# Kernel optimization log

Hardware: AMD Instinct MI355X
Metric: run time of the kernel (lower is better)

Reference implementation:

```python
import jax, jax.numpy as jnp
import numpy as np

EPS = 1e-5
B, S, D = 4, 2048, 128
BALL_SCALE = 0.05  # keeps points inside the unit Poincare ball for c=1


def setup_inputs() -> dict:
    key = jax.random.key(0)
    kq, kk, kv = jax.random.split(key, 3)
    q = jax.random.normal(kq, (B, S, D), dtype=jnp.float32) * BALL_SCALE
    k = jax.random.normal(kk, (B, S, D), dtype=jnp.float32) * BALL_SCALE
    v_tangent = jax.random.normal(kv, (B, S, D), dtype=jnp.float32)
    c = jnp.asarray(1.0, dtype=jnp.float32)
    beta = jnp.asarray(0.0, dtype=jnp.float32)            # nn.Parameter init 0.0
    attention_bias = jnp.asarray(0.0, dtype=jnp.float32)  # nn.Parameter init 0.0
    return {"q": q, "k": k, "v_tangent": v_tangent, "c": c,
            "beta": beta, "attention_bias": attention_bias}


def reference(q, k, v_tangent, c, beta, attention_bias):
    sqrt_c = jnp.sqrt(c)

    # --- pairwise Poincare distance (all fp32, as in the torch autocast block) ---
    x_norm_sq = jnp.sum(q * q, axis=-1, keepdims=True)            # (B,S,1)
    y_norm_sq = jnp.sum(k * k, axis=-1, keepdims=True)            # (B,S,1)
    xy_dot = jnp.einsum('bsd,btd->bst', q, k)                     # (B,S,S)
    y_norm_sq_t = jnp.swapaxes(y_norm_sq, -2, -1)                 # (B,1,S)
    diff_norm_sq = x_norm_sq - 2.0 * xy_dot + y_norm_sq_t         # ||x-y||^2, (B,S,S)
    denom = (1.0 - c * x_norm_sq) * (1.0 - c * y_norm_sq_t)       # (B,S,S)
    arg = 1.0 + 2.0 * c * diff_norm_sq / jnp.maximum(denom, EPS)
    dist = jnp.arccosh(jnp.maximum(arg, 1.0 + EPS)) / sqrt_c      # (B,S,S)

    # --- attention ---
    beta_positive = jax.nn.softplus(beta)
    attention_scores = -beta_positive * dist - attention_bias
    attention_weights = jax.nn.softmax(attention_scores, axis=-1)  # (B,S,S)
    output_tangent = jnp.einsum('bst,btd->bsd', attention_weights, v_tangent)

    # --- exp map at origin ---
    v_norm = jnp.maximum(
        jnp.sqrt(jnp.sum(output_tangent * output_tangent, axis=-1, keepdims=True)), EPS)
    output_hyperbolic = (jnp.tanh(sqrt_c * v_norm) / sqrt_c) * (output_tangent / v_norm)

    return output_hyperbolic, attention_weights
```

## Files before the change

kernel.cpp:

```cpp
#include <hip/hip_runtime.h>
#include <math.h>

#define B_ 4
#define S_ 2048
#define D_ 128
#define EPSF 1e-5f
#define BN 128
#define PSB 272
#define PRS 4112

typedef __attribute__((ext_vector_type(8))) short short8;
typedef __attribute__((ext_vector_type(4))) float f32x4;

static __device__ __forceinline__ unsigned short f2bf(float f) {
    unsigned u = __float_as_uint(f);
    return (unsigned short)((u + 0x7fffu + ((u >> 16) & 1u)) >> 16);
}


__global__ __launch_bounds__(256) void convqk_kernel(const float* __restrict__ q,
                                                     const float* __restrict__ k,
                                                     const float* __restrict__ cp,
                                                     float* __restrict__ qn, float* __restrict__ kn,
                                                     float* __restrict__ lws,
                                                     float2* __restrict__ qng, float2* __restrict__ kng,
                                                     unsigned* __restrict__ Qb, unsigned* __restrict__ Kb) {
    int row = blockIdx.x * 4 + (threadIdx.x >> 6);
    int lane = threadIdx.x & 63;
    const int NR = B_ * S_;
    const float cc = cp[0];
    bool isQ = row < NR;
    int r = isQ ? row : row - NR;
    float2 v = ((const float2*)(isQ ? q : k))[(size_t)r * 64 + lane];
    unsigned pk = (unsigned)f2bf(v.x) | ((unsigned)f2bf(v.y) << 16);
    float nrm = v.x * v.x + v.y * v.y;
#pragma unroll
    for (int m = 1; m <= 32; m <<= 1) nrm += __shfl_xor(nrm, m, 64);
    if (isQ) {
        Qb[(size_t)r * 64 + lane] = pk;
        if (lane == 0) {
            qn[r] = nrm;
            qng[r] = make_float2(nrm, 2.f * cc * __builtin_amdgcn_rcpf(1.f - cc * nrm));
        }
        if (lane == 1) lws[r] = 0.f;
    } else {
        int c = lane >> 2;
        int cs = c ^ (r & 7);
        Kb[(size_t)r * 64 + cs * 4 + (lane & 3)] = pk;
        if (lane == 0) {
            kn[r] = nrm;
            kng[r] = make_float2(nrm, __builtin_amdgcn_rcpf(1.f - cc * nrm));
        }
    }
}

__global__ __launch_bounds__(256) void convv_kernel(const float* __restrict__ v, uint4* __restrict__ Vtb) {
    __shared__ unsigned short Vs[128 * 132];
    int b = blockIdx.x >> 4;
    int t = blockIdx.x & 15;
    int tid = threadIdx.x;
    const float* src = v + ((size_t)b * S_ + t * 128) * D_;
    int d4 = tid & 31, key0 = tid >> 5;
#pragma unroll
    for (int it = 0; it < 16; ++it) {
        int key = key0 + it * 8;
        float4 f = *(const float4*)(src + (size_t)key * D_ + d4 * 4);
        unsigned short* dst = &Vs[key * 132 + d4 * 4];
        dst[0] = f2bf(f.x); dst[1] = f2bf(f.y); dst[2] = f2bf(f.z); dst[3] = f2bf(f.w);
    }
    __syncthreads();
    uint4* tile = Vtb + (size_t)blockIdx.x * (128 * 16);
    int d = tid & 127;
    int cl = tid >> 7;
#pragma unroll
    for (int it = 0; it < 8; ++it) {
        int c = cl + it * 2;
        int kb = c * 8;
        unsigned short e0 = Vs[(kb + 0) * 132 + d], e1 = Vs[(kb + 1) * 132 + d];
        unsigned short e2 = Vs[(kb + 2) * 132 + d], e3 = Vs[(kb + 3) * 132 + d];
        unsigned short e4 = Vs[(kb + 4) * 132 + d], e5 = Vs[(kb + 5) * 132 + d];
        unsigned short e6 = Vs[(kb + 6) * 132 + d], e7 = Vs[(kb + 7) * 132 + d];
        uint4 o;
        o.x = (unsigned)e0 | ((unsigned)e1 << 16);
        o.y = (unsigned)e2 | ((unsigned)e3 << 16);
        o.z = (unsigned)e4 | ((unsigned)e5 << 16);
        o.w = (unsigned)e6 | ((unsigned)e7 << 16);
        tile[d * 16 + (c ^ (d & 7))] = o;
    }
}


__global__ __launch_bounds__(1024, 4) void hattn6_kernel(
    const unsigned short* __restrict__ Qb, const char* __restrict__ Kb, const char* __restrict__ Vtb,
    const float2* __restrict__ qng, const float2* __restrict__ kng,
    const float* __restrict__ cp, const float* __restrict__ betap, const float* __restrict__ biasp,
    float* __restrict__ hout, float* __restrict__ wout) {

    __shared__ __align__(1024) char smem[132096];
    float* l_row = (float*)(smem + 131840);
    float* nsq_s = (float*)(smem + 131968);

    const int tid = threadIdx.x;
    const int lane = tid & 63, wave = tid >> 6;
    const int wm = wave & 1, wn = wave >> 1;
    const int lm = lane & 15, quad = lane >> 4;

    int xcd = blockIdx.x & 7;
    int b = xcd >> 1;
    int rb = (blockIdx.x >> 3) * 2 + (xcd & 1);
    int s0 = rb * 32;
    const size_t bS = (size_t)b * S_;

    const float beta = betap[0], bias = biasp[0];
    const float cc = cp[0];
    const float beta_pos = fmaxf(beta, 0.f) + log1pf(__expf(-fabsf(beta)));
    const float sqrt_c = sqrtf(cc);
    const float bneg = -beta_pos / sqrt_c;
    const float bias2 = -bias * 1.442695040888963f;
    const float onepe = 1.f + EPSF;

    const char* KbBase = Kb + bS * 256;
    const char* VtBase = Vtb + (size_t)b * 16 * 32768;

    if (tid < 32) {
        float2 x = qng[bS + s0 + tid];
        *(float2*)(smem + 131584 + tid * 8) = x;
    } else if (tid < 64) {
        l_row[tid - 32] = 0.f;
    } else if (tid < 96) {
        nsq_s[tid - 64] = 0.f;
    }

    const int n0 = wn * 16 + lm;
    short8 kf[4];
    float2 yg;
    {
        const char* kb0 = KbBase + n0 * 256;
#pragma unroll
        for (int ks = 0; ks < 4; ++ks) {
            int c = ks * 4 + quad;
            kf[ks] = *(const short8*)(kb0 + ((c ^ (n0 & 7)) * 16));
        }
        yg = kng[bS + n0];
    }

    short8 aq[4];
    {
        const unsigned short* qrow = Qb + (bS + s0 + wm * 16 + lm) * D_;
#pragma unroll
        for (int ks = 0; ks < 4; ++ks)
            aq[ks] = *(const short8*)(qrow + ks * 32 + quad * 8);
    }

    __syncthreads();

    float2 xr4[4];
#pragma unroll
    for (int r = 0; r < 4; ++r)
        xr4[r] = *(const float2*)(smem + 131584 + (wm * 16 + quad * 4 + r) * 8);

    f32x4 o = {0.f, 0.f, 0.f, 0.f};
    float lacc[4] = {0.f, 0.f, 0.f, 0.f};

    for (int it = 0; it < 16; ++it) {
        f32x4 acc = {0.f, 0.f, 0.f, 0.f};
#pragma unroll
        for (int ks = 0; ks < 4; ++ks)
            acc = __builtin_amdgcn_mfma_f32_16x16x32_bf16(aq[ks], kf[ks], acc, 0, 0, 0);

        short8 kfn[4];
        float2 ygn;
        if (it < 15) {
            const char* kb = KbBase + (size_t)(it + 1) * 32768 + n0 * 256;
#pragma unroll
            for (int ks = 0; ks < 4; ++ks) {
                int c = ks * 4 + quad;
                kfn[ks] = *(const short8*)(kb + ((c ^ (n0 & 7)) * 16));
            }
            ygn = kng[bS + (size_t)(it + 1) * 128 + n0];
        }

        short8 vf[4];
        {
            const char* vb = VtBase + (size_t)it * 32768 + n0 * 256;
#pragma unroll
            for (int ks = 0; ks < 4; ++ks) {
                int c = ks * 4 + quad;
                vf[ks] = *(const short8*)(vb + ((c ^ (n0 & 7)) * 16));
            }
        }

#pragma unroll
        for (int r = 0; r < 4; ++r) {
            int row = wm * 16 + quad * 4 + r;
            float diff = fmaf(-2.f, acc[r], xr4[r].x + yg.x);
            float arg = fmaf(diff * yg.y, xr4[r].y, 1.f);
            arg = fmaxf(arg, onepe);
            float w = arg + sqrtf(fmaf(arg, arg, -1.f));
            float pv = __builtin_amdgcn_exp2f(fmaf(bneg, __builtin_amdgcn_logf(w), bias2));
            *(unsigned short*)(smem + row * PRS + (it * 128 + n0) * 2) = f2bf(pv);
            lacc[r] += pv;
        }
        __syncthreads();

        {
            const char* prow = smem + (wm * 16 + lm) * PRS + it * 256 + quad * 16;
#pragma unroll
            for (int ks = 0; ks < 4; ++ks) {
                short8 ap = *(const short8*)(prow + ks * 64);
                o = __builtin_amdgcn_mfma_f32_16x16x32_bf16(ap, vf[ks], o, 0, 0, 0);
            }
        }

        if (it < 15) {
#pragma unroll
            for (int ks = 0; ks < 4; ++ks) kf[ks] = kfn[ks];
            yg = ygn;
        }
    }

#pragma unroll
    for (int r = 0; r < 4; ++r) {
        float s = lacc[r];
#pragma unroll
        for (int m = 1; m <= 8; m <<= 1) s += __shfl_xor(s, m, 64);
        if (lm == 0) atomicAdd(&l_row[wm * 16 + quad * 4 + r], s);
    }
    __syncthreads();

    float linv[4];
#pragma unroll
    for (int r = 0; r < 4; ++r) linv[r] = 1.f / l_row[wm * 16 + quad * 4 + r];

#pragma unroll
    for (int r = 0; r < 4; ++r) {
        float x = o[r] * linv[r];
        o[r] = x;
        float np = x * x;
#pragma unroll
        for (int m = 1; m <= 8; m <<= 1) np += __shfl_xor(np, m, 64);
        if (lm == 0) atomicAdd(&nsq_s[wm * 16 + quad * 4 + r], np);
    }
    __syncthreads();
#pragma unroll
    for (int r = 0; r < 4; ++r) {
        int row = wm * 16 + quad * 4 + r;
        float vn = fmaxf(sqrtf(nsq_s[row]), EPSF);
        float a = sqrt_c * vn;
        float th = 1.f - 2.f / (__expf(2.f * a) + 1.f);
        float sc = th / a;
        hout[(bS + s0 + row) * D_ + n0] = o[r] * sc;
    }

    {
        float4* wdst = (float4*)(wout + (bS + s0) * (size_t)S_);
#pragma unroll
        for (int j = 0; j < 8; ++j) {
            int idx = tid + j * 1024;
            int row = idx >> 8;
            int ch = idx & 255;
            float lr = 1.f / l_row[row];
            uint4 u = *(const uint4*)(smem + row * PRS + ch * 16);
            float4 f0, f1;
            f0.x = __uint_as_float(u.x << 16) * lr;
            f0.y = __uint_as_float(u.x & 0xffff0000u) * lr;
            f0.z = __uint_as_float(u.y << 16) * lr;
            f0.w = __uint_as_float(u.y & 0xffff0000u) * lr;
            f1.x = __uint_as_float(u.z << 16) * lr;
            f1.y = __uint_as_float(u.z & 0xffff0000u) * lr;
            f1.z = __uint_as_float(u.w << 16) * lr;
            f1.w = __uint_as_float(u.w & 0xffff0000u) * lr;
            wdst[idx * 2] = f0;
            wdst[idx * 2 + 1] = f1;
        }
    }
}


__global__ __launch_bounds__(512, 2) void hattn_kernel(
    const unsigned short* __restrict__ Qb, const char* __restrict__ Kb, const char* __restrict__ Vtb,
    const float* __restrict__ qn, const float* __restrict__ kn,
    const float* __restrict__ cp, const float* __restrict__ betap, const float* __restrict__ biasp,
    float* __restrict__ lws, float* __restrict__ houtg, float* __restrict__ woutg) {

    __shared__ __align__(1024) char smem[75136];
    char* KsB = smem;
    char* VtB = smem + 32768;
    char* PsB = smem + 65536;
    float* kn_s  = (float*)(smem + 74240);
    float* qn_s  = (float*)(smem + 74752);
    float* l_row = (float*)(smem + 74880);
    float* nsq_s = (float*)(smem + 75008);

    const int tid = threadIdx.x;
    const int lane = tid & 63, wave = tid >> 6;
    const int wm = wave & 1, wn = wave >> 1;
    const int lm = lane & 15, quad = lane >> 4;

    int xcd = blockIdx.x & 7;
    int b = xcd >> 1;
    int rb = (blockIdx.x >> 3) * 2 + (xcd & 1);
    int s0 = rb * 32;
    const size_t bS = (size_t)b * S_;

    const float cc = cp[0], beta = betap[0], bias = biasp[0];
    const float beta_pos = fmaxf(beta, 0.f) + log1pf(__expf(-fabsf(beta)));
    const float sqrt_c = sqrtf(cc);
    const float inv_sqrt_c = 1.f / sqrt_c;

    if (tid < 32) {
        qn_s[tid] = qn[bS + s0 + tid];
        l_row[tid] = 0.f;
        nsq_s[tid] = 0.f;
    }

    short8 aq[4];
    {
        const unsigned short* qrow = Qb + (bS + s0 + wm * 16 + lm) * D_;
#pragma unroll
        for (int ks = 0; ks < 4; ++ks)
            aq[ks] = *(const short8*)(qrow + ks * 32 + quad * 8);
    }

    f32x4 o0 = {0.f, 0.f, 0.f, 0.f}, o1 = {0.f, 0.f, 0.f, 0.f};

    const char* KbBase = Kb + bS * 256;
    const char* VtBase = Vtb + (size_t)b * 16 * 32768;

    for (int t = 0; t < S_ / BN; ++t) {
        int t0 = t * BN;
        __syncthreads();
        {
            const uint4* ksrc = (const uint4*)(KbBase + (size_t)t0 * 256);
            const uint4* vsrc = (const uint4*)(VtBase + (size_t)t * 32768);
            uint4* kd = (uint4*)KsB;
            uint4* vd = (uint4*)VtB;
#pragma unroll
            for (int i = 0; i < 4; ++i) {
                kd[tid + i * 512] = ksrc[tid + i * 512];
                vd[tid + i * 512] = vsrc[tid + i * 512];
            }
            if (tid < BN) kn_s[tid] = kn[bS + t0 + tid];
        }
        __syncthreads();

        f32x4 acc0 = {0.f, 0.f, 0.f, 0.f}, acc1 = {0.f, 0.f, 0.f, 0.f};
#pragma unroll
        for (int ks = 0; ks < 4; ++ks) {
            int n0 = wn * 32 + lm;
            int c = ks * 4 + quad;
            short8 b0 = *(const short8*)(KsB + n0 * 256 + ((c ^ (n0 & 7)) * 16));
            int n1 = n0 + 16;
            short8 b1 = *(const short8*)(KsB + n1 * 256 + ((c ^ (n1 & 7)) * 16));
            acc0 = __builtin_amdgcn_mfma_f32_16x16x32_bf16(aq[ks], b0, acc0, 0, 0, 0);
            acc1 = __builtin_amdgcn_mfma_f32_16x16x32_bf16(aq[ks], b1, acc1, 0, 0, 0);
        }

        float lp[4];
#pragma unroll
        for (int r = 0; r < 4; ++r) {
            int row = wm * 16 + quad * 4 + r;
            float xn = qn_s[row];
            float fx = 1.f - cc * xn;
            float p0, p1;
#pragma unroll
            for (int nt = 0; nt < 2; ++nt) {
                int col = wn * 32 + nt * 16 + lm;
                float dot = (nt == 0) ? acc0[r] : acc1[r];
                float yn = kn_s[col];
                float diff = xn - 2.f * dot + yn;
                float den = fmaxf(fx * (1.f - cc * yn), EPSF);
                float arg = fmaf(2.f * cc * diff, __builtin_amdgcn_rcpf(den), 1.f);
                arg = fmaxf(arg, 1.f + EPSF);
                float dist = __logf(arg + sqrtf(arg * arg - 1.f)) * inv_sqrt_c;
                float p = __expf(fmaf(-beta_pos, dist, -bias));
                woutg[(bS + s0 + row) * S_ + t0 + col] = p;
                *(unsigned short*)(PsB + row * PSB + col * 2) = f2bf(p);
                if (nt == 0) p0 = p; else p1 = p;
            }
            lp[r] = p0 + p1;
        }
#pragma unroll
        for (int r = 0; r < 4; ++r) {
            float s = lp[r];
#pragma unroll
            for (int m = 1; m <= 8; m <<= 1) s += __shfl_xor(s, m, 64);
            if (lm == 0) atomicAdd(&l_row[wm * 16 + quad * 4 + r], s);
        }
        __syncthreads();

#pragma unroll
        for (int ks = 0; ks < 4; ++ks) {
            short8 ap = *(const short8*)(PsB + (wm * 16 + lm) * PSB + (ks * 32 + quad * 8) * 2);
            int d0 = wn * 32 + lm;
            int c = ks * 4 + quad;
            short8 v0 = *(const short8*)(VtB + d0 * 256 + ((c ^ (d0 & 7)) * 16));
            int d1 = d0 + 16;
            short8 v1 = *(const short8*)(VtB + d1 * 256 + ((c ^ (d1 & 7)) * 16));
            o0 = __builtin_amdgcn_mfma_f32_16x16x32_bf16(ap, v0, o0, 0, 0, 0);
            o1 = __builtin_amdgcn_mfma_f32_16x16x32_bf16(ap, v1, o1, 0, 0, 0);
        }
    }
    __syncthreads();

    float xs0[4], xs1[4];
#pragma unroll
    for (int r = 0; r < 4; ++r) {
        int row = wm * 16 + quad * 4 + r;
        float linv = __builtin_amdgcn_rcpf(l_row[row]);
        float x0 = o0[r] * linv, x1 = o1[r] * linv;
        xs0[r] = x0; xs1[r] = x1;
        float np = x0 * x0 + x1 * x1;
#pragma unroll
        for (int m = 1; m <= 8; m <<= 1) np += __shfl_xor(np, m, 64);
        if (lm == 0) atomicAdd(&nsq_s[row], np);
    }
    if (tid < 32) lws[bS + s0 + tid] = l_row[tid];
    __syncthreads();
#pragma unroll
    for (int r = 0; r < 4; ++r) {
        int row = wm * 16 + quad * 4 + r;
        float vn = fmaxf(sqrtf(nsq_s[row]), EPSF);
        float a = sqrt_c * vn;
        float th = 1.f - 2.f * __builtin_amdgcn_rcpf(__expf(2.f * a) + 1.f);
        float sc = th / a;
        houtg[(bS + s0 + row) * D_ + wn * 32 + lm] = xs0[r] * sc;
        houtg[(bS + s0 + row) * D_ + wn * 32 + 16 + lm] = xs1[r] * sc;
    }
}

__global__ __launch_bounds__(256) void wnorm_kernel(float* __restrict__ w,
                                                    const float* __restrict__ lws) {
    size_t idx = (size_t)blockIdx.x * 256 + threadIdx.x;
    int row = (int)(idx >> 9);
    float linv = 1.f / lws[row];
    float4* p = (float4*)w + idx;
    float4 v = *p;
    v.x *= linv; v.y *= linv; v.z *= linv; v.w *= linv;
    *p = v;
}


extern "C" void kernel_launch(void* const* d_in, const int* in_sizes, int n_in,
                              void* d_out, int out_size, void* d_ws, size_t ws_size,
                              hipStream_t stream) {
    const float* q    = (const float*)d_in[0];
    const float* k    = (const float*)d_in[1];
    const float* v    = (const float*)d_in[2];
    const float* c    = (const float*)d_in[3];
    const float* beta = (const float*)d_in[4];
    const float* ab   = (const float*)d_in[5];

    float* out  = (float*)d_out;
    float* hout = out;
    float* wout = out + (size_t)B_ * S_ * D_;

    float* qn  = (float*)d_ws;
    float* kn  = qn + B_ * S_;
    float* lws = kn + B_ * S_;
    char*  wsb = (char*)d_ws;
    const size_t QG_OFF = 98304;
    const size_t KG_OFF = QG_OFF + 65536;
    const size_t QB_OFF = KG_OFF + 65536;
    const size_t KB_OFF = QB_OFF + 2097152;
    const size_t VT_OFF = KB_OFF + 2097152;
    const size_t NEED1  = VT_OFF + 2097152;

    float2*  qng = (float2*)(wsb + QG_OFF);
    float2*  kng = (float2*)(wsb + KG_OFF);
    unsigned* Qb = (unsigned*)(wsb + QB_OFF);
    unsigned* Kb = (unsigned*)(wsb + KB_OFF);
    uint4*   Vtb = (uint4*)(wsb + VT_OFF);

    if (ws_size >= NEED1) {
        convqk_kernel<<<4096, 256, 0, stream>>>(q, k, c, qn, kn, lws, qng, kng, Qb, Kb);
        convv_kernel<<<64, 256, 0, stream>>>(v, Vtb);
        hattn6_kernel<<<256, 1024, 0, stream>>>((const unsigned short*)Qb, (const char*)Kb,
                                                (const char*)Vtb, qng, kng, c, beta, ab,
                                                hout, wout);
    } else {
        convqk_kernel<<<4096, 256, 0, stream>>>(q, k, c, qn, kn, lws, qng, kng, Qb, Kb);
        convv_kernel<<<64, 256, 0, stream>>>(v, Vtb);
        hattn_kernel<<<256, 512, 0, stream>>>((const unsigned short*)Qb, (const char*)Kb,
                                              (const char*)Vtb, qn, kn, c, beta, ab,
                                              lws, hout, wout);
        wnorm_kernel<<<(B_ * S_ * S_ / 4) / 256, 256, 0, stream>>>(wout, lws);
    }
}
```

Measured before the change: 136.8 us.

## Re-layout K and V bf16 tiles into k-slice-major order for coalesced fragment loads

Changes the workspace layout of the bf16 K and transposed V tiles from XOR-swizzled rows to a k-slice-major layout (ks*8192 + n*64 + quad*16), so each wave's MFMA fragment loads hit contiguous 1 KB segments instead of strided 256-byte rows. It also hoists the V and next-K global loads to the top of the loop behind a sched_barrier so they issue before the QK MFMAs, and pads the P row stride in shared memory. The fallback kernel is updated to match the new layout. The intent is to cut global-load transaction count and latency in the main attention kernel, at the cost of higher register pressure from the early loads.

```diff
diff --git a/kernel.cpp b/kernel.cpp
--- a/kernel.cpp
+++ b/kernel.cpp
@@ -7,7 +7,7 @@
 #define EPSF 1e-5f
 #define BN 128
 #define PSB 272
-#define PRS 4112
+#define PRS 4128
 
 typedef __attribute__((ext_vector_type(8))) short short8;
 typedef __attribute__((ext_vector_type(4))) float f32x4;
@@ -44,9 +44,10 @@
         }
         if (lane == 1) lws[r] = 0.f;
     } else {
-        int c = lane >> 2;
-        int cs = c ^ (r & 7);
-        Kb[(size_t)r * 64 + cs * 4 + (lane & 3)] = pk;
+        int b = r >> 11, rbk = r & 2047;
+        int tile = rbk >> 7, n = rbk & 127;
+        Kb[(size_t)b * 131072 + tile * 8192 + (lane >> 4) * 2048 + n * 16 +
+           ((lane >> 2) & 3) * 4 + (lane & 3)] = pk;
         if (lane == 0) {
             kn[r] = nrm;
             kng[r] = make_float2(nrm, __builtin_amdgcn_rcpf(1.f - cc * nrm));
@@ -85,20 +86,20 @@
         o.y = (unsigned)e2 | ((unsigned)e3 << 16);
         o.z = (unsigned)e4 | ((unsigned)e5 << 16);
         o.w = (unsigned)e6 | ((unsigned)e7 << 16);
-        tile[d * 16 + (c ^ (d & 7))] = o;
-    }
-}
-
-
-__global__ __launch_bounds__(1024, 4) void hattn6_kernel(
+        tile[(c >> 2) * 512 + d * 4 + (c & 3)] = o;
+    }
+}
+
+
+__global__ __launch_bounds__(1024, 4) void hattn7_kernel(
     const unsigned short* __restrict__ Qb, const char* __restrict__ Kb, const char* __restrict__ Vtb,
     const float2* __restrict__ qng, const float2* __restrict__ kng,
     const float* __restrict__ cp, const float* __restrict__ betap, const float* __restrict__ biasp,
     float* __restrict__ hout, float* __restrict__ wout) {
 
-    __shared__ __align__(1024) char smem[132096];
-    float* l_row = (float*)(smem + 131840);
-    float* nsq_s = (float*)(smem + 131968);
+    __shared__ __align__(1024) char smem[132608];
+    float* l_row = (float*)(smem + 132352);
+    float* nsq_s = (float*)(smem + 132480);
 
     const int tid = threadIdx.x;
     const int lane = tid & 63, wave = tid >> 6;
@@ -119,12 +120,12 @@
     const float bias2 = -bias * 1.442695040888963f;
     const float onepe = 1.f + EPSF;
 
-    const char* KbBase = Kb + bS * 256;
+    const char* KbBase = Kb + (size_t)b * 524288;
     const char* VtBase = Vtb + (size_t)b * 16 * 32768;
 
     if (tid < 32) {
         float2 x = qng[bS + s0 + tid];
-        *(float2*)(smem + 131584 + tid * 8) = x;
+        *(float2*)(smem + 132096 + tid * 8) = x;
     } else if (tid < 64) {
         l_row[tid - 32] = 0.f;
     } else if (tid < 96) {
@@ -132,15 +133,13 @@
     }
 
     const int n0 = wn * 16 + lm;
+    const int foff = n0 * 64 + quad * 16;
     short8 kf[4];
     float2 yg;
     {
-        const char* kb0 = KbBase + n0 * 256;
-#pragma unroll
-        for (int ks = 0; ks < 4; ++ks) {
-            int c = ks * 4 + quad;
-            kf[ks] = *(const short8*)(kb0 + ((c ^ (n0 & 7)) * 16));
-        }
+#pragma unroll
+        for (int ks = 0; ks < 4; ++ks)
+            kf[ks] = *(const short8*)(KbBase + ks * 8192 + foff);
         yg = kng[bS + n0];
     }
 
@@ -157,38 +156,33 @@
     float2 xr4[4];
 #pragma unroll
     for (int r = 0; r < 4; ++r)
-        xr4[r] = *(const float2*)(smem + 131584 + (wm * 16 + quad * 4 + r) * 8);
+        xr4[r] = *(const float2*)(smem + 132096 + (wm * 16 + quad * 4 + r) * 8);
 
     f32x4 o = {0.f, 0.f, 0.f, 0.f};
     float lacc[4] = {0.f, 0.f, 0.f, 0.f};
 
     for (int it = 0; it < 16; ++it) {
+        short8 kfn[4], vf[4];
+        float2 ygn;
+        {
+            const char* vb = VtBase + (size_t)it * 32768 + foff;
+#pragma unroll
+            for (int ks = 0; ks < 4; ++ks)
+                vf[ks] = *(const short8*)(vb + ks * 8192);
+        }
+        if (it < 15) {
+            const char* kb = KbBase + (size_t)(it + 1) * 32768 + foff;
+#pragma unroll
+            for (int ks = 0; ks < 4; ++ks)
+                kfn[ks] = *(const short8*)(kb + ks * 8192);
+            ygn = kng[bS + (size_t)(it + 1) * 128 + n0];
+        }
+        __builtin_amdgcn_sched_barrier(0);
+
         f32x4 acc = {0.f, 0.f, 0.f, 0.f};
 #pragma unroll
         for (int ks = 0; ks < 4; ++ks)
             acc = __builtin_amdgcn_mfma_f32_16x16x32_bf16(aq[ks], kf[ks], acc, 0, 0, 0);
-
-        short8 kfn[4];
-        float2 ygn;
-        if (it < 15) {
-            const char* kb = KbBase + (size_t)(it + 1) * 32768 + n0 * 256;
-#pragma unroll
-            for (int ks = 0; ks < 4; ++ks) {
-                int c = ks * 4 + quad;
-                kfn[ks] = *(const short8*)(kb + ((c ^ (n0 & 7)) * 16));
-            }
-            ygn = kng[bS + (size_t)(it + 1) * 128 + n0];
-        }
-
-        short8 vf[4];
-        {
-            const char* vb = VtBase + (size_t)it * 32768 + n0 * 256;
-#pragma unroll
-            for (int ks = 0; ks < 4; ++ks) {
-                int c = ks * 4 + quad;
-                vf[ks] = *(const short8*)(vb + ((c ^ (n0 & 7)) * 16));
-            }
-        }
 
 #pragma unroll
         for (int r = 0; r < 4; ++r) {
@@ -324,14 +318,14 @@
 
     f32x4 o0 = {0.f, 0.f, 0.f, 0.f}, o1 = {0.f, 0.f, 0.f, 0.f};
 
-    const char* KbBase = Kb + bS * 256;
+    const char* KbBase = Kb + (size_t)b * 524288;
     const char* VtBase = Vtb + (size_t)b * 16 * 32768;
 
     for (int t = 0; t < S_ / BN; ++t) {
         int t0 = t * BN;
         __syncthreads();
         {
-            const uint4* ksrc = (const uint4*)(KbBase + (size_t)t0 * 256);
+            const uint4* ksrc = (const uint4*)(KbBase + (size_t)t * 32768);
             const uint4* vsrc = (const uint4*)(VtBase + (size_t)t * 32768);
             uint4* kd = (uint4*)KsB;
             uint4* vd = (uint4*)VtB;
@@ -344,14 +338,12 @@
         }
         __syncthreads();
 
+        int n0 = wn * 32 + lm;
         f32x4 acc0 = {0.f, 0.f, 0.f, 0.f}, acc1 = {0.f, 0.f, 0.f, 0.f};
 #pragma unroll
         for (int ks = 0; ks < 4; ++ks) {
-            int n0 = wn * 32 + lm;
-            int c = ks * 4 + quad;
-            short8 b0 = *(const short8*)(KsB + n0 * 256 + ((c ^ (n0 & 7)) * 16));
-            int n1 = n0 + 16;
-            short8 b1 = *(const short8*)(KsB + n1 * 256 + ((c ^ (n1 & 7)) * 16));
+            short8 b0 = *(const short8*)(KsB + ks * 8192 + n0 * 64 + quad * 16);
+            short8 b1 = *(const short8*)(KsB + ks * 8192 + (n0 + 16) * 64 + quad * 16);
             acc0 = __builtin_amdgcn_mfma_f32_16x16x32_bf16(aq[ks], b0, acc0, 0, 0, 0);
             acc1 = __builtin_amdgcn_mfma_f32_16x16x32_bf16(aq[ks], b1, acc1, 0, 0, 0);
         }
@@ -393,10 +385,8 @@
         for (int ks = 0; ks < 4; ++ks) {
             short8 ap = *(const short8*)(PsB + (wm * 16 + lm) * PSB + (ks * 32 + quad * 8) * 2);
             int d0 = wn * 32 + lm;
-            int c = ks * 4 + quad;
-            short8 v0 = *(const short8*)(VtB + d0 * 256 + ((c ^ (d0 & 7)) * 16));
-            int d1 = d0 + 16;
-            short8 v1 = *(const short8*)(VtB + d1 * 256 + ((c ^ (d1 & 7)) * 16));
+            short8 v0 = *(const short8*)(VtB + ks * 8192 + d0 * 64 + quad * 16);
+            short8 v1 = *(const short8*)(VtB + ks * 8192 + (d0 + 16) * 64 + quad * 16);
             o0 = __builtin_amdgcn_mfma_f32_16x16x32_bf16(ap, v0, o0, 0, 0, 0);
             o1 = __builtin_amdgcn_mfma_f32_16x16x32_bf16(ap, v1, o1, 0, 0, 0);
         }
@@ -475,7 +465,7 @@
     if (ws_size >= NEED1) {
         convqk_kernel<<<4096, 256, 0, stream>>>(q, k, c, qn, kn, lws, qng, kng, Qb, Kb);
         convv_kernel<<<64, 256, 0, stream>>>(v, Vtb);
-        hattn6_kernel<<<256, 1024, 0, stream>>>((const unsigned short*)Qb, (const char*)Kb,
+        hattn7_kernel<<<256, 1024, 0, stream>>>((const unsigned short*)Qb, (const char*)Kb,
                                                 (const char*)Vtb, qng, kng, c, beta, ab,
                                                 hout, wout);
     } else {
```

Measured after the change: 137.6 us. Within noise of the previous version (+0.6%).
